# Optimization experiments

Hardware: AMD Instinct MI355X
Metric: run time of the kernel (lower is better)

## Reference

```python
import jax, jax.numpy as jnp
import numpy as np

B, T = 64, 512
E, F, NUM = 8, 64, 16          # num embedding features, per-feature emb dim, numeric feats
D = E * F + NUM                 # 528, input_dim
HE = 512                        # encoder_hidden
HD = 512                        # decoder_gru_hidden
V = 500                         # vocab per categorical feature


def setup_inputs() -> dict:
    key = jax.random.key(0)
    ks = jax.random.split(key, 32)
    se = 1.0 / np.sqrt(HE)
    sd = 1.0 / np.sqrt(HD)
    u = lambda k, shape, s: jax.random.uniform(k, shape, jnp.float32, -s, s)
    return dict(
        x=jax.random.normal(ks[0], (B, T, D), jnp.float32),
        # encoder nn.GRU params (gate order r,z,n)
        Wih=u(ks[1], (3 * HE, D), se), Whh=u(ks[2], (3 * HE, HE), se),
        bih=u(ks[3], (3 * HE,), se), bhh=u(ks[4], (3 * HE,), se),
        # decoder layer 0 (input_size=D)
        W0x=u(ks[5], (3 * HD, D), sd), b0x=u(ks[6], (3 * HD,), sd),
        W0h=u(ks[7], (3 * HD, HD), sd), b0h=u(ks[8], (3 * HD,), sd),
        W0m=u(ks[9], (HD, HE + HD), sd), b0m=u(ks[10], (HD,), sd),
        # decoder layer 1 (input_size=HD)
        W1x=u(ks[11], (3 * HD, HD), sd), b1x=u(ks[12], (3 * HD,), sd),
        W1h=u(ks[13], (3 * HD, HD), sd), b1h=u(ks[14], (3 * HD,), sd),
        W1m=u(ks[15], (HD, HE + HD), sd), b1m=u(ks[16], (HD,), sd),
        # output heads
        Wout=u(ks[17], (D, HD), sd), bout=u(ks[18], (D,), sd),
        Wdel=u(ks[19], (1, HD), sd), bdel=u(ks[20], (1,), sd),
        # stacked per-feature vocab heads: Linear(F, V) for each of E features
        Wemb=u(ks[21], (E, V, F), 1.0 / np.sqrt(F)), bemb=u(ks[22], (E, V), 1.0 / np.sqrt(F)),
        seq_lens=jax.random.randint(ks[23], (B,), 1, T + 1),
    )


def _gru_cell(xg, hg, hx):
    # xg, hg: [B, 3H] precomputed input/hidden projections; hx: mixed hidden
    xr, xz, xn = jnp.split(xg, 3, axis=-1)
    hr, hz, hn = jnp.split(hg, 3, axis=-1)
    r = jax.nn.sigmoid(xr + hr)
    z = jax.nn.sigmoid(xz + hz)
    n = jnp.tanh(xn + r * hn)
    return z * hx + (1.0 - z) * n  # custom GRUCell convention: hy = z*hx + (1-z)*n


def reference(x, Wih, Whh, bih, bhh, W0x, b0x, W0h, b0h, W0m, b0m,
              W1x, b1x, W1h, b1h, W1m, b1m, Wout, bout, Wdel, bdel,
              Wemb, bemb, seq_lens):
    Bc, Tc, Dc = x.shape
    # ---------------- encoder: standard nn.GRU ----------------
    xg_enc = jnp.einsum('btd,gd->tbg', x, Wih) + bih  # [T,B,3HE]

    def enc_step(h, xt):
        hg = h @ Whh.T + bhh
        xr, xz, xn = jnp.split(xt, 3, axis=-1)
        hr, hz, hn = jnp.split(hg, 3, axis=-1)
        r = jax.nn.sigmoid(xr + hr)
        z = jax.nn.sigmoid(xz + hz)
        n = jnp.tanh(xn + r * hn)
        h = (1.0 - z) * n + z * h  # torch nn.GRU convention
        return h, h

    _, hs = jax.lax.scan(enc_step, jnp.zeros((Bc, HE), x.dtype), xg_enc)  # hs: [T,B,HE]
    lens = jnp.clip(seq_lens - 1, 0, Tc - 1)
    last_hidden = hs[lens, jnp.arange(Bc)]  # == all_hid[:, lens].diagonal().T -> [B,HE]

    # ---------------- DecoderGRU with per-step global mixing ----------------
    x2h0 = jnp.einsum('btd,gd->tbg', x, W0x) + b0x  # [T,B,3HD]
    # mix_global(cat([global_hidden, hx])) : global part is constant over time
    ghm0 = last_hidden @ W0m[:, :HE].T + b0m  # [B,HD]
    ghm1 = last_hidden @ W1m[:, :HE].T + b1m
    W0mh = W0m[:, HE:]
    W1mh = W1m[:, HE:]

    def dec_step(carry, xg_t):
        h0, h1 = carry
        hx0 = ghm0 + h0 @ W0mh.T
        h0 = _gru_cell(xg_t, hx0 @ W0h.T + b0h, hx0)
        xg1 = h0 @ W1x.T + b1x
        hx1 = ghm1 + h1 @ W1mh.T
        h1 = _gru_cell(xg1, hx1 @ W1h.T + b1h, hx1)
        return (h0, h1), h1

    z0 = jnp.zeros((Bc, HD), x.dtype)
    _, dec = jax.lax.scan(dec_step, (z0, z0), x2h0)  # [T,B,HD]
    dec = dec.transpose(1, 0, 2)  # [B,T,HD]

    out = (dec @ Wout.T + bout)[:, :-1, :]              # [B,T-1,D]
    pred_delta = (dec @ Wdel.T + bdel)[:, :-1, 0]       # [B,T-1]
    resized = out[:, :, :E * F].reshape(Bc, Tc - 1, E, F)
    emb_logits = jnp.einsum('btef,evf->ebtv', resized, Wemb) + bemb[:, None, None, :]
    return out, pred_delta, emb_logits, last_hidden
```

## Files before the change

kernel.cpp:

```cpp
#include <hip/hip_runtime.h>
#include <stdint.h>

typedef unsigned short u16;
typedef __attribute__((ext_vector_type(8))) short short8;
typedef __attribute__((ext_vector_type(4))) float f32x4;

#define MFMA16(a,b,c) __builtin_amdgcn_mfma_f32_16x16x32_bf16((a),(b),(c),0,0,0)
#define AT_LD(p)    __hip_atomic_load((p), __ATOMIC_RELAXED, __HIP_MEMORY_SCOPE_AGENT)
#define AT_LD64(p)  __hip_atomic_load((p), __ATOMIC_RELAXED, __HIP_MEMORY_SCOPE_AGENT)
#define AT_ST(p,v)  __hip_atomic_store((p), (v), __ATOMIC_RELAXED, __HIP_MEMORY_SCOPE_AGENT)

__device__ __forceinline__ float b2f(u16 u){
  union { uint32_t i; float f; } v; v.i = ((uint32_t)u) << 16; return v.f;
}
__device__ __forceinline__ u16 f2bf(float f){
  union { float f; uint32_t i; } v; v.f = f;
  uint32_t x = v.i;
  return (u16)((x + 0x7fffu + ((x >> 16) & 1u)) >> 16);
}
__device__ __forceinline__ float sigm(float x){ return 1.f/(1.f + __expf(-x)); }
__device__ __forceinline__ float tanh_f(float x){ float e = __expf(-2.f*x); return 2.f/(1.f+e) - 1.f; }

__device__ __forceinline__ void gbar_arrive(unsigned* flags, int my, unsigned target){
  __syncthreads();
  if (threadIdx.x == 0) AT_ST(&flags[my*32], target);
}
__device__ __forceinline__ void gbar_wait16(unsigned* flags, unsigned target){
  if (threadIdx.x < 16){
    while (AT_LD(&flags[threadIdx.x*32]) < target) {}
  }
  __syncthreads();
}

__device__ __forceinline__ f32x4 xpose4(f32x4 a, int m){
  int b0 = m & 1, b1 = (m >> 1) & 1;
  float s01 = b0 ? a[0] : a[1];
  float s23 = b0 ? a[2] : a[3];
  float r01 = __shfl_xor(s01, 1);
  float r23 = __shfl_xor(s23, 1);
  float w0 = b0 ? r01 : a[0];
  float w1 = b0 ? a[1] : r01;
  float w2 = b0 ? r23 : a[2];
  float w3 = b0 ? a[3] : r23;
  float u02 = b1 ? w0 : w2;
  float u13 = b1 ? w1 : w3;
  float p02 = __shfl_xor(u02, 2);
  float p13 = __shfl_xor(u13, 2);
  f32x4 x;
  x[0] = b1 ? p02 : w0;
  x[1] = b1 ? p13 : w1;
  x[2] = b1 ? w2 : p02;
  x[3] = b1 ? w3 : p13;
  return x;
}

__device__ __forceinline__ void stage_h512(const u16* hrd, u16* hs, int tid){
  const unsigned long long* h64 = (const unsigned long long*)hrd;
  #pragma unroll
  for (int cc=0; cc<8; ++cc){
    int S = cc*512 + tid;
    int row = S >> 6, s = S & 63;
    union { unsigned long long q[2]; short8 v; } pk;
    pk.q[0] = AT_LD64(h64 + (size_t)S*2);
    pk.q[1] = AT_LD64(h64 + (size_t)S*2 + 1);
    *(short8*)&hs[row*512 + ((s ^ (row&7))<<3)] = pk.v;
  }
}
__device__ __forceinline__ void stage_h256(const u16* hrd, u16* hs, int tid){
  const unsigned long long* h64 = (const unsigned long long*)hrd;
  #pragma unroll
  for (int cc=0; cc<16; ++cc){
    int S = cc*256 + tid;
    int row = S >> 6, s = S & 63;
    union { unsigned long long q[2]; short8 v; } pk;
    pk.q[0] = AT_LD64(h64 + (size_t)S*2);
    pk.q[1] = AT_LD64(h64 + (size_t)S*2 + 1);
    *(short8*)&hs[row*512 + ((s ^ (row&7))<<3)] = pk.v;
  }
}

__global__ void cvt_pad(const float* __restrict__ src, u16* __restrict__ dst,
                        int R, int sStride, int sOff, int Cd, int Ccopy){
  int i = blockIdx.x*256 + threadIdx.x;
  if (i >= R*Cd) return;
  int r = i / Cd, c = i % Cd;
  dst[i] = (c < Ccopy) ? f2bf(src[(size_t)r*sStride + sOff + c]) : (u16)0;
}

__global__ void padf(const float* __restrict__ src, float* __restrict__ dst, int R, int Cs, int Cd){
  int i = blockIdx.x*256 + threadIdx.x;
  if (i >= R*Cd) return;
  int r = i/Cd, c = i%Cd;
  dst[i] = (c < Cs) ? src[r*Cs + c] : 0.f;
}

__global__ void wmT_kernel(const float* __restrict__ Wm, u16* __restrict__ dst){
  int idx = blockIdx.x*256 + threadIdx.x;
  if (idx >= 512*512) return;
  int j = idx >> 9, k = idx & 511;
  dst[idx] = f2bf(Wm[(size_t)k*1024 + 512 + j]);
}

__global__ __launch_bounds__(256) void gemm_bt(
    const u16* __restrict__ A, int lda,
    const u16* __restrict__ Bw, int ldb,
    const float* __restrict__ bias,
    int M, int N, int K, int mode,
    void* __restrict__ o0, void* __restrict__ o1, void* __restrict__ o2, int ldo)
{
  if (mode == 3){
    int e = blockIdx.z;
    A    += (size_t)e * 64;
    Bw   += (size_t)e * 512 * 64;
    bias += (size_t)e * 512;
  }
  __shared__ u16 As[128*64];
  __shared__ u16 Bs[128*64];
  const int row0 = blockIdx.x * 128, col0 = blockIdx.y * 128;
  const int tid = threadIdx.x;
  const int l = tid & 63, w = tid >> 6;
  const int lr = l & 15, lk = l >> 4;
  const int wr = w >> 1, wc = w & 1;
  f32x4 acc[4][4];
  #pragma unroll
  for (int a=0;a<4;++a)
    #pragma unroll
    for (int b=0;b<4;++b) acc[a][b] = (f32x4){0.f,0.f,0.f,0.f};

  for (int k0 = 0; k0 < K; k0 += 64){
    #pragma unroll
    for (int s = 0; s < 4; ++s){
      int cid = s*256 + tid;
      int r = cid >> 3, ck = cid & 7;
      *(short8*)&As[r*64 + ck*8] = *(const short8*)&A[(size_t)(row0 + r)*lda + k0 + ck*8];
      *(short8*)&Bs[r*64 + ck*8] = *(const short8*)&Bw[(size_t)(col0 + r)*ldb + k0 + ck*8];
    }
    __syncthreads();
    #pragma unroll
    for (int kt = 0; kt < 2; ++kt){
      short8 af[4], bf[4];
      #pragma unroll
      for (int mt=0;mt<4;++mt) af[mt] = *(const short8*)&As[(wr*64 + mt*16 + lr)*64 + kt*32 + lk*8];
      #pragma unroll
      for (int nt=0;nt<4;++nt) bf[nt] = *(const short8*)&Bs[(wc*64 + nt*16 + lr)*64 + kt*32 + lk*8];
      #pragma unroll
      for (int mt=0;mt<4;++mt)
        #pragma unroll
        for (int nt=0;nt<4;++nt) acc[mt][nt] = MFMA16(af[mt], bf[nt], acc[mt][nt]);
    }
    __syncthreads();
  }

  #pragma unroll
  for (int mt=0;mt<4;++mt){
    #pragma unroll
    for (int nt=0;nt<4;++nt){
      int col = col0 + wc*64 + nt*16 + lr;
      float bv = bias[col];
      #pragma unroll
      for (int i=0;i<4;++i){
        int r = row0 + wr*64 + mt*16 + lk*4 + i;
        float v = acc[mt][nt][i] + bv;
        if (mode == 0){
          int bb = r >> 9, t = r & 511;
          size_t ro = ((size_t)t*64 + bb)*1536;
          if (col < 1536) ((u16*)o0)[ro + col] = f2bf(v);
          else            ((u16*)o1)[ro + col - 1536] = f2bf(v);
        } else if (mode == 1){
          ((u16*)o0)[(size_t)r*ldo + col] = f2bf(v);
        } else if (mode == 2){
          int t = r >> 6, bb = r & 63;
          if (t < 511){
            size_t orow = (size_t)bb*511 + t;
            if (col < 512){
              ((float*)o0)[orow*528 + col] = v;
              ((u16*)o2)[orow*512 + col] = f2bf(v);
            } else if (col < 528){
              ((float*)o0)[orow*528 + col] = v;
            } else if (col == 528){
              ((float*)o1)[orow] = v;
            }
          }
        } else if (mode == 3){
          if (r < M && col < 500) ((float*)o0)[(size_t)(blockIdx.z)*16352000ull + (size_t)r*500 + col] = v;
        } else {
          if (r < M) ((float*)o0)[(size_t)r*ldo + col] = v;
        }
      }
    }
  }
}

__global__ __launch_bounds__(512,2) void enc_kernel(
    const u16* __restrict__ Whh, const float* __restrict__ bhh,
    const u16* __restrict__ XGE, const int* __restrict__ seqs,
    u16* __restrict__ hd, float* __restrict__ lasth,
    unsigned* __restrict__ flags)
{
  __shared__ u16 hs[64*512];
  const int tid = threadIdx.x;
  const int l = tid & 63, w = tid >> 6;
  const int lr = l & 15, lk = l >> 4;
  const int m = l & 3;
  const int gw = blockIdx.x*8 + w;
  const int hcol = gw*4 + (lr >> 2);

  const int msel = (m == 3) ? 0 : m;
  const u16* wbase = Whh + ((size_t)(msel*512) + hcol)*512;
  short8 bw[16];
  #pragma unroll
  for (int kt=0;kt<16;++kt) bw[kt] = *(const short8*)&wbase[kt*32 + lk*8];

  const float bhr = bhh[hcol], bhz = bhh[512+hcol], bhn = bhh[1024+hcol];
  int rowc[4]; int len[4]; float hreg[4];
  float xr[4], xz[4], xn[4];
  #pragma unroll
  for (int c=0;c<4;++c){
    rowc[c] = c*16 + lk*4 + m;
    len[c] = seqs[rowc[c]];
    hreg[c] = 0.f;
    const u16* p = XGE + (size_t)rowc[c]*1536;
    xr[c]=b2f(p[hcol]); xz[c]=b2f(p[512+hcol]); xn[c]=b2f(p[1024+hcol]);
  }

  for (int t=0; t<512; ++t){
    const u16* hrd = hd + (t & 1)*32768;
    u16*       hwr = hd + ((t & 1)^1)*32768;
    stage_h512(hrd, hs, tid);
    __syncthreads();
    #pragma unroll
    for (int c=0;c<4;++c){
      short8 af[16];
      #pragma unroll
      for (int kt=0;kt<16;++kt)
        af[kt] = *(const short8*)&hs[(c*16+lr)*512 + (((kt*4+lk) ^ (lr&7))<<3)];
      f32x4 acc = (f32x4){0.f,0.f,0.f,0.f};
      #pragma unroll
      for (int kt=0;kt<16;++kt) acc = MFMA16(af[kt], bw[kt], acc);
      f32x4 x = xpose4(acc, m);
      float rg = sigm(xr[c] + x[0] + bhr);
      float zg = sigm(xz[c] + x[1] + bhz);
      float ng = tanh_f(xn[c] + rg*(x[2] + bhn));
      float hv = (1.f - zg)*ng + zg*hreg[c];
      hreg[c] = hv;
      AT_ST(&hwr[rowc[c]*512 + hcol], f2bf(hv));
      if (t == len[c]-1) lasth[rowc[c]*512 + hcol] = hv;
    }
    if (t < 511){
      gbar_arrive(flags, blockIdx.x, (unsigned)(t+1));
      const u16* xgn = XGE + (size_t)(t+1)*98304;
      #pragma unroll
      for (int c=0;c<4;++c){
        const u16* p = xgn + (size_t)rowc[c]*1536;
        xr[c]=b2f(p[hcol]); xz[c]=b2f(p[512+hcol]); xn[c]=b2f(p[1024+hcol]);
      }
      gbar_wait16(flags, (unsigned)(t+1));
    }
  }
}

__global__ __launch_bounds__(256,1) void decf_kernel(
    const u16* __restrict__ Wm0, const u16* __restrict__ Wcp0,
    const float* __restrict__ ghm0v, const float* __restrict__ ghW0v,
    const u16* __restrict__ W1xc, const float* __restrict__ b1xv,
    const u16* __restrict__ Wm1, const u16* __restrict__ Wcp1,
    const float* __restrict__ ghm1v, const float* __restrict__ ghW1v,
    const u16* __restrict__ XG0,
    u16* __restrict__ h0d, u16* __restrict__ h1d,
    u16* __restrict__ xgb,
    u16* __restrict__ Hall,
    unsigned* __restrict__ flags)
{
  __shared__ u16 hs[64*512];
  const int tid = threadIdx.x;
  const int l = tid & 63, w = tid >> 6;
  const int lr = l & 15, lk = l >> 4;
  const int m = l & 3;
  const int role1 = (blockIdx.x >= 32) ? 1 : 0;
  const int b = blockIdx.x & 31;
  const int gw = b*4 + w;
  const int hcol = gw*4 + (lr >> 2);

  const u16* Wm  = role1 ? Wm1  : Wm0;
  const u16* Wcp = role1 ? Wcp1 : Wcp0;
  const float* ghm = role1 ? ghm1v : ghm0v;
  const float* ghW = role1 ? ghW1v : ghW0v;

  const u16* wb = (m == 0) ? (Wm + (size_t)hcol*512)
                           : (Wcp + ((size_t)((m-1)*512) + hcol)*512);
  short8 bw[16];
  #pragma unroll
  for (int kt=0;kt<16;++kt) bw[kt] = *(const short8*)&wb[kt*32 + lk*8];

  const bool xact = (!role1) && (gw < 96);
  const int xcol0 = gw*16;
  const int cbase = xcol0 + (lr & ~3);
  short8 bwx[16];
  float bx0=0.f, bx1=0.f, bx2=0.f, bx3=0.f;
  if (xact){
    #pragma unroll
    for (int kt=0;kt<16;++kt) bwx[kt] = *(const short8*)&W1xc[(size_t)(xcol0+lr)*512 + kt*32 + lk*8];
    bx0 = b1xv[cbase]; bx1 = b1xv[cbase+1]; bx2 = b1xv[cbase+2]; bx3 = b1xv[cbase+3];
  }

  int rowc[4]; float ghmr[4], g0[4], g1[4], g2[4];
  #pragma unroll
  for (int c=0;c<4;++c){
    int row = c*16 + lk*4 + m; rowc[c] = row;
    ghmr[c] = ghm[row*512 + hcol];
    g0[c] = ghW[row*1536 + hcol];
    g1[c] = ghW[row*1536 + 512 + hcol];
    g2[c] = ghW[row*1536 + 1024 + hcol];
  }
  float xr[4], xz[4], xn[4];
  if (!role1){
    #pragma unroll
    for (int c=0;c<4;++c){
      const u16* p = XG0 + (size_t)rowc[c]*1536;
      xr[c]=b2f(p[hcol]); xz[c]=b2f(p[512+hcol]); xn[c]=b2f(p[1024+hcol]);
    }
  } else {
    #pragma unroll
    for (int c=0;c<4;++c){ xr[c]=0.f; xz[c]=0.f; xn[c]=0.f; }
  }

  for (int p=0; p<=513; ++p){
    if (!role1){
      if (p <= 512){
        const int sp = p & 1;
        const u16* hrd = h0d + sp*32768;
        u16*       hwr = h0d + (sp^1)*32768;
        stage_h256(hrd, hs, tid);
        __syncthreads();
        #pragma unroll
        for (int c=0;c<4;++c){
          short8 af[16];
          #pragma unroll
          for (int kt=0;kt<16;++kt)
            af[kt] = *(const short8*)&hs[(c*16+lr)*512 + (((kt*4+lk) ^ (lr&7))<<3)];
          if (p <= 511){
            f32x4 ga = (f32x4){0.f,0.f,0.f,0.f};
            #pragma unroll
            for (int kt=0;kt<16;++kt) ga = MFMA16(af[kt], bw[kt], ga);
            f32x4 x = xpose4(ga, m);
            float hx = x[0] + ghmr[c];
            float rv = sigm(xr[c] + x[1] + g0[c]);
            float zv = sigm(xz[c] + x[2] + g1[c]);
            float nv = tanh_f(xn[c] + rv*(x[3] + g2[c]));
            float hv = zv*hx + (1.f - zv)*nv;
            AT_ST(&hwr[rowc[c]*512 + hcol], f2bf(hv));
          }
          if (p >= 1 && xact){
            u16* xw = xgb + (size_t)((p-1)%3)*98304;
            f32x4 xa = (f32x4){0.f,0.f,0.f,0.f};
            #pragma unroll
            for (int kt=0;kt<16;++kt) xa = MFMA16(af[kt], bwx[kt], xa);
            f32x4 xv = xpose4(xa, m);
            unsigned lo = (unsigned)f2bf(xv[0]+bx0) | ((unsigned)f2bf(xv[1]+bx1) << 16);
            unsigned hi = (unsigned)f2bf(xv[2]+bx2) | ((unsigned)f2bf(xv[3]+bx3) << 16);
            unsigned long long v64 = (unsigned long long)lo | ((unsigned long long)hi << 32);
            __hip_atomic_store((unsigned long long*)&xw[(size_t)rowc[c]*1536 + cbase], v64,
                               __ATOMIC_RELAXED, __HIP_MEMORY_SCOPE_AGENT);
          }
        }
      }
    } else {
      if (p >= 2){
        const int t = p - 2;
        const u16* xb = xgb + (size_t)(t%3)*98304;
        #pragma unroll
        for (int c=0;c<4;++c){
          xr[c] = b2f(AT_LD(&xb[(size_t)rowc[c]*1536 + hcol]));
          xz[c] = b2f(AT_LD(&xb[(size_t)rowc[c]*1536 + 512 + hcol]));
          xn[c] = b2f(AT_LD(&xb[(size_t)rowc[c]*1536 + 1024 + hcol]));
        }
        const u16* hrd = h1d + (t&1)*32768;
        u16*       hwr = h1d + ((t&1)^1)*32768;
        stage_h256(hrd, hs, tid);
        __syncthreads();
        #pragma unroll
        for (int c=0;c<4;++c){
          short8 af[16];
          #pragma unroll
          for (int kt=0;kt<16;++kt)
            af[kt] = *(const short8*)&hs[(c*16+lr)*512 + (((kt*4+lk) ^ (lr&7))<<3)];
          f32x4 ga = (f32x4){0.f,0.f,0.f,0.f};
          #pragma unroll
          for (int kt=0;kt<16;++kt) ga = MFMA16(af[kt], bw[kt], ga);
          f32x4 x = xpose4(ga, m);
          float hx = x[0] + ghmr[c];
          float rv = sigm(xr[c] + x[1] + g0[c]);
          float zv = sigm(xz[c] + x[2] + g1[c]);
          float nv = tanh_f(xn[c] + rv*(x[3] + g2[c]));
          float hv = zv*hx + (1.f - zv)*nv;
          u16 hb = f2bf(hv);
          AT_ST(&hwr[rowc[c]*512 + hcol], hb);
          Hall[(size_t)t*32768 + rowc[c]*512 + hcol] = hb;
        }
      }
    }
    if (p < 513){
      __syncthreads();
      if (tid == 0) AT_ST(&flags[blockIdx.x*32], (unsigned)(p+1));
      if (!role1 && p <= 510){
        const u16* xgn = XG0 + (size_t)(p+1)*98304;
        #pragma unroll
        for (int c=0;c<4;++c){
          const u16* q = xgn + (size_t)rowc[c]*1536;
          xr[c]=b2f(q[hcol]); xz[c]=b2f(q[512+hcol]); xn[c]=b2f(q[1024+hcol]);
        }
      }
      if (!role1){
        if (tid < 32){
          while (AT_LD(&flags[tid*32]) < (unsigned)(p+1)) {}
        } else if (tid < 64){
          if (p >= 1){ while (AT_LD(&flags[tid*32]) < (unsigned)p) {} }
        }
      } else {
        if (tid < 64){
          while (AT_LD(&flags[tid*32]) < (unsigned)(p+1)) {}
        }
      }
      __syncthreads();
    }
  }
}

__global__ void ghm_kernel(const float* __restrict__ lasth,
                           const float* __restrict__ W0m, const float* __restrict__ b0m,
                           const float* __restrict__ W1m, const float* __restrict__ b1m,
                           float* __restrict__ ghm0, float* __restrict__ ghm1,
                           u16* __restrict__ ghmP)
{
  int idx = blockIdx.x*256 + threadIdx.x;
  int chain = idx >> 15;
  int j = (idx >> 6) & 511;
  int b = idx & 63;
  const float* Wm = chain ? W1m : W0m;
  const float* bm = chain ? b1m : b0m;
  float s = 0.f;
  for (int k=0;k<512;++k) s += lasth[b*512 + k] * Wm[(size_t)j*1024 + k];
  float v = s + bm[j];
  (chain ? ghm1 : ghm0)[b*512 + j] = v;
  ghmP[(size_t)chain*65536 + b*512 + j] = f2bf(v);
}

extern "C" void kernel_launch(void* const* d_in, const int* in_sizes, int n_in,
                              void* d_out, int out_size, void* d_ws, size_t ws_size,
                              hipStream_t stream)
{
  const float* x    = (const float*)d_in[0];
  const float* Wih  = (const float*)d_in[1];
  const float* Whh  = (const float*)d_in[2];
  const float* bih  = (const float*)d_in[3];
  const float* bhh  = (const float*)d_in[4];
  const float* W0x  = (const float*)d_in[5];
  const float* b0x  = (const float*)d_in[6];
  const float* W0h  = (const float*)d_in[7];
  const float* b0h  = (const float*)d_in[8];
  const float* W0m  = (const float*)d_in[9];
  const float* b0m  = (const float*)d_in[10];
  const float* W1x  = (const float*)d_in[11];
  const float* b1x  = (const float*)d_in[12];
  const float* W1h  = (const float*)d_in[13];
  const float* b1h  = (const float*)d_in[14];
  const float* W1m  = (const float*)d_in[15];
  const float* b1m  = (const float*)d_in[16];
  const float* Wout = (const float*)d_in[17];
  const float* bout = (const float*)d_in[18];
  const float* Wdel = (const float*)d_in[19];
  const float* bdel = (const float*)d_in[20];
  const float* Wemb = (const float*)d_in[21];
  const float* bemb = (const float*)d_in[22];
  const int*   seqs = (const int*)d_in[23];
  float* out = (float*)d_out;

  const size_t OFF_DELTA = 17267712ull;
  const size_t OFF_EMB   = 17300416ull;
  const size_t OFF_LASTH = 148116416ull;

  uint8_t* ws = (uint8_t*)d_ws;
  size_t off = 0;
  auto alloc = [&](size_t bytes)->size_t{ size_t p = off; off += (bytes + 511) & ~(size_t)511; return p; };
  u16*   XGE  = (u16*)(ws + alloc(32768ull*1536*2));
  u16*   WmT0 = XGE;
  u16*   WmT1 = XGE + 262144;
  u16*   XG0  = (u16*)(ws + alloc(32768ull*1536*2));
  u16*   Ob   = XG0;
  uint8_t* reg3 = ws + alloc(2ull*33554432);
  u16*   Xp   = (u16*)reg3;
  u16*   H1   = (u16*)reg3;
  u16*   Wc   = (u16*)(ws + alloc(3072ull*576*2));
  u16*   Whc  = (u16*)(ws + alloc(1536ull*512*2));
  u16*   W0hc = (u16*)(ws + alloc(1536ull*512*2));
  u16*   W1hc = (u16*)(ws + alloc(1536ull*512*2));
  u16*   W1xc = (u16*)(ws + alloc(1536ull*512*2));
  u16*   Wm0c = (u16*)(ws + alloc(512ull*512*2));
  u16*   Wm1c = (u16*)(ws + alloc(512ull*512*2));
  u16*   Wcp0 = (u16*)(ws + alloc(1536ull*512*2));
  u16*   Wcp1 = (u16*)(ws + alloc(1536ull*512*2));
  u16*   Woc  = (u16*)(ws + alloc(640ull*512*2));
  u16*   Wep  = (u16*)(ws + alloc(8ull*512*64*2));
  u16*   ghmP = (u16*)(ws + alloc(2ull*128*512*2));
  u16*   xgb  = (u16*)(ws + alloc(3ull*64*1536*2));
  float* bc1  = (float*)(ws + alloc(3072*4));
  float* bc3  = (float*)(ws + alloc(640*4));
  float* bep  = (float*)(ws + alloc(8*512*4));
  float* bzero= (float*)(ws + alloc(512*4));
  float* ghm0 = (float*)(ws + alloc(64*512*4));
  float* ghm1 = (float*)(ws + alloc(64*512*4));
  float* ghW0 = (float*)(ws + alloc(64*1536*4));
  float* ghW1 = (float*)(ws + alloc(64*1536*4));
  size_t state_off = off;
  u16*   henc = (u16*)(ws + alloc(2*64*512*2));
  u16*   h0d  = (u16*)(ws + alloc(2*64*512*2));
  u16*   h1d  = (u16*)(ws + alloc(2*64*512*2));
  unsigned* bars = (unsigned*)(ws + alloc(16384));
  size_t state_bytes = off - state_off;
  if (ws_size < off) return;

  hipMemsetAsync(ws + state_off, 0, state_bytes, stream);
  hipMemsetAsync(Woc, 0, 640ull*512*2, stream);
  hipMemsetAsync(Wep, 0, 8ull*512*64*2, stream);
  hipMemsetAsync(ghmP, 0, 2ull*128*512*2, stream);
  hipMemsetAsync(bc3, 0, 640*4, stream);
  hipMemsetAsync(bzero, 0, 512*4, stream);

  hipMemcpyAsync(bc1,        bih,  1536*4, hipMemcpyDeviceToDevice, stream);
  hipMemcpyAsync(bc1 + 1536, b0x,  1536*4, hipMemcpyDeviceToDevice, stream);
  hipMemcpyAsync(bc3,        bout, 528*4,  hipMemcpyDeviceToDevice, stream);
  hipMemcpyAsync(bc3 + 528,  bdel, 4,      hipMemcpyDeviceToDevice, stream);

  auto CV = [&](const float* s, u16* d, int R, int sStride, int sOff, int Cd, int Ccopy){
    int total = R*Cd; int gb = (total + 255)/256;
    cvt_pad<<<dim3(gb), dim3(256), 0, stream>>>(s, d, R, sStride, sOff, Cd, Ccopy);
  };
  CV(x,    Xp, 32768, 528, 0, 576, 528);
  CV(Wih,  Wc,              1536, 528, 0, 576, 528);
  CV(W0x,  Wc + 1536ull*576,1536, 528, 0, 576, 528);
  CV(Whh,  Whc,  1536, 512, 0, 512, 512);
  CV(W0h,  W0hc, 1536, 512, 0, 512, 512);
  CV(W1h,  W1hc, 1536, 512, 0, 512, 512);
  CV(W1x,  W1xc, 1536, 512, 0, 512, 512);
  CV(W0m,  Wm0c, 512, 1024, 512, 512, 512);
  CV(W1m,  Wm1c, 512, 1024, 512, 512, 512);
  CV(Wout, Woc,              528, 512, 0, 512, 512);
  CV(Wdel, Woc + 528ull*512, 1,   512, 0, 512, 512);
  for (int e=0;e<8;++e) CV(Wemb + (size_t)e*32000, Wep + (size_t)e*32768, 500, 64, 0, 64, 64);
  {
    int gb = (8*512 + 255)/256;
    padf<<<dim3(gb), dim3(256), 0, stream>>>(bemb, bep, 8, 500, 512);
  }
  wmT_kernel<<<dim3(1024), dim3(256), 0, stream>>>(W0m, WmT0);
  wmT_kernel<<<dim3(1024), dim3(256), 0, stream>>>(W1m, WmT1);

  gemm_bt<<<dim3(12,4), dim3(256), 0, stream>>>(W0hc, 512, WmT0, 512, bzero,
      1536, 512, 512, 1, Wcp0, nullptr, nullptr, 512);
  gemm_bt<<<dim3(12,4), dim3(256), 0, stream>>>(W1hc, 512, WmT1, 512, bzero,
      1536, 512, 512, 1, Wcp1, nullptr, nullptr, 512);

  gemm_bt<<<dim3(256,24), dim3(256), 0, stream>>>(Xp, 576, Wc, 576, bc1,
      32768, 3072, 576, 0, XGE, XG0, nullptr, 0);
  enc_kernel<<<dim3(16), dim3(512), 0, stream>>>(Whc, bhh, XGE, seqs,
      henc, out + OFF_LASTH, bars + 0);
  ghm_kernel<<<dim3(256), dim3(256), 0, stream>>>(out + OFF_LASTH, W0m, b0m, W1m, b1m,
      ghm0, ghm1, ghmP);
  gemm_bt<<<dim3(1,12), dim3(256), 0, stream>>>(ghmP, 512, W0hc, 512, b0h,
      64, 1536, 512, 5, ghW0, nullptr, nullptr, 1536);
  gemm_bt<<<dim3(1,12), dim3(256), 0, stream>>>(ghmP + 65536, 512, W1hc, 512, b1h,
      64, 1536, 512, 5, ghW1, nullptr, nullptr, 1536);
  decf_kernel<<<dim3(64), dim3(256), 0, stream>>>(
      Wm0c, Wcp0, ghm0, ghW0, W1xc, b1x,
      Wm1c, Wcp1, ghm1, ghW1,
      XG0, h0d, h1d, xgb, H1, bars + 1024);
  gemm_bt<<<dim3(256,5), dim3(256), 0, stream>>>(H1, 512, Woc, 512, bc3,
      32768, 640, 512, 2, out, out + OFF_DELTA, Ob, 0);
  gemm_bt<<<dim3(256,4,8), dim3(256), 0, stream>>>(Ob, 512, Wep, 64, bep,
      32704, 512, 64, 3, out + OFF_EMB, nullptr, nullptr, 0);
}
```

Before: 8.276 ms.

## Overlap decoder input projection GEMM with encoder recurrence; shrink layer-1 decoder blocks

The decoder layer-0 input projection (XG0) is split out of the big input GEMM and computed by extra blocks launched alongside the 16 persistent encoder recurrence blocks in one kernel. This lets that GEMM run on otherwise idle CUs while the latency-bound encoder loop runs. Separately, the decoder layer-1 role now uses 16 blocks that each handle two hidden-column groups instead of 32 blocks handling one, so the barrier covers 48 blocks instead of 64. The xgb ring-buffer index is also re-expressed. The risk is that the GEMM blocks may be scheduled ahead of the encoder blocks or compete with them for resources, and that layer-1 blocks now do twice the work per step.

```diff
diff --git a/kernel.cpp b/kernel.cpp
--- a/kernel.cpp
+++ b/kernel.cpp
@@ -191,70 +191,133 @@
   }
 }
 
-__global__ __launch_bounds__(512,2) void enc_kernel(
+__global__ __launch_bounds__(512,2) void encg_kernel(
     const u16* __restrict__ Whh, const float* __restrict__ bhh,
     const u16* __restrict__ XGE, const int* __restrict__ seqs,
     u16* __restrict__ hd, float* __restrict__ lasth,
-    unsigned* __restrict__ flags)
+    unsigned* __restrict__ flags,
+    const u16* __restrict__ Xp, const u16* __restrict__ Wcx,
+    const float* __restrict__ biasx, u16* __restrict__ XG0)
 {
-  __shared__ u16 hs[64*512];
+  __shared__ u16 shbuf[64*512];
   const int tid = threadIdx.x;
-  const int l = tid & 63, w = tid >> 6;
-  const int lr = l & 15, lk = l >> 4;
-  const int m = l & 3;
-  const int gw = blockIdx.x*8 + w;
-  const int hcol = gw*4 + (lr >> 2);
-
-  const int msel = (m == 3) ? 0 : m;
-  const u16* wbase = Whh + ((size_t)(msel*512) + hcol)*512;
-  short8 bw[16];
-  #pragma unroll
-  for (int kt=0;kt<16;++kt) bw[kt] = *(const short8*)&wbase[kt*32 + lk*8];
-
-  const float bhr = bhh[hcol], bhz = bhh[512+hcol], bhn = bhh[1024+hcol];
-  int rowc[4]; int len[4]; float hreg[4];
-  float xr[4], xz[4], xn[4];
-  #pragma unroll
-  for (int c=0;c<4;++c){
-    rowc[c] = c*16 + lk*4 + m;
-    len[c] = seqs[rowc[c]];
-    hreg[c] = 0.f;
-    const u16* p = XGE + (size_t)rowc[c]*1536;
-    xr[c]=b2f(p[hcol]); xz[c]=b2f(p[512+hcol]); xn[c]=b2f(p[1024+hcol]);
-  }
-
-  for (int t=0; t<512; ++t){
-    const u16* hrd = hd + (t & 1)*32768;
-    u16*       hwr = hd + ((t & 1)^1)*32768;
-    stage_h512(hrd, hs, tid);
-    __syncthreads();
+  if (blockIdx.x < 16){
+    u16* hs = shbuf;
+    const int l = tid & 63, w = tid >> 6;
+    const int lr = l & 15, lk = l >> 4;
+    const int m = l & 3;
+    const int gw = blockIdx.x*8 + w;
+    const int hcol = gw*4 + (lr >> 2);
+
+    const int msel = (m == 3) ? 0 : m;
+    const u16* wbase = Whh + ((size_t)(msel*512) + hcol)*512;
+    short8 bw[16];
+    #pragma unroll
+    for (int kt=0;kt<16;++kt) bw[kt] = *(const short8*)&wbase[kt*32 + lk*8];
+
+    const float bhr = bhh[hcol], bhz = bhh[512+hcol], bhn = bhh[1024+hcol];
+    int rowc[4]; int len[4]; float hreg[4];
+    float xr[4], xz[4], xn[4];
     #pragma unroll
     for (int c=0;c<4;++c){
-      short8 af[16];
-      #pragma unroll
-      for (int kt=0;kt<16;++kt)
-        af[kt] = *(const short8*)&hs[(c*16+lr)*512 + (((kt*4+lk) ^ (lr&7))<<3)];
-      f32x4 acc = (f32x4){0.f,0.f,0.f,0.f};
-      #pragma unroll
-      for (int kt=0;kt<16;++kt) acc = MFMA16(af[kt], bw[kt], acc);
-      f32x4 x = xpose4(acc, m);
-      float rg = sigm(xr[c] + x[0] + bhr);
-      float zg = sigm(xz[c] + x[1] + bhz);
-      float ng = tanh_f(xn[c] + rg*(x[2] + bhn));
-      float hv = (1.f - zg)*ng + zg*hreg[c];
-      hreg[c] = hv;
-      AT_ST(&hwr[rowc[c]*512 + hcol], f2bf(hv));
-      if (t == len[c]-1) lasth[rowc[c]*512 + hcol] = hv;
-    }
-    if (t < 511){
-      gbar_arrive(flags, blockIdx.x, (unsigned)(t+1));
-      const u16* xgn = XGE + (size_t)(t+1)*98304;
+      rowc[c] = c*16 + lk*4 + m;
+      len[c] = seqs[rowc[c]];
+      hreg[c] = 0.f;
+      const u16* p = XGE + (size_t)rowc[c]*1536;
+      xr[c]=b2f(p[hcol]); xz[c]=b2f(p[512+hcol]); xn[c]=b2f(p[1024+hcol]);
+    }
+
+    for (int t=0; t<512; ++t){
+      const u16* hrd = hd + (t & 1)*32768;
+      u16*       hwr = hd + ((t & 1)^1)*32768;
+      stage_h512(hrd, hs, tid);
+      __syncthreads();
       #pragma unroll
       for (int c=0;c<4;++c){
-        const u16* p = xgn + (size_t)rowc[c]*1536;
-        xr[c]=b2f(p[hcol]); xz[c]=b2f(p[512+hcol]); xn[c]=b2f(p[1024+hcol]);
-      }
-      gbar_wait16(flags, (unsigned)(t+1));
+        short8 af[16];
+        #pragma unroll
+        for (int kt=0;kt<16;++kt)
+          af[kt] = *(const short8*)&hs[(c*16+lr)*512 + (((kt*4+lk) ^ (lr&7))<<3)];
+        f32x4 acc = (f32x4){0.f,0.f,0.f,0.f};
+        #pragma unroll
+        for (int kt=0;kt<16;++kt) acc = MFMA16(af[kt], bw[kt], acc);
+        f32x4 x = xpose4(acc, m);
+        float rg = sigm(xr[c] + x[0] + bhr);
+        float zg = sigm(xz[c] + x[1] + bhz);
+        float ng = tanh_f(xn[c] + rg*(x[2] + bhn));
+        float hv = (1.f - zg)*ng + zg*hreg[c];
+        hreg[c] = hv;
+        AT_ST(&hwr[rowc[c]*512 + hcol], f2bf(hv));
+        if (t == len[c]-1) lasth[rowc[c]*512 + hcol] = hv;
+      }
+      if (t < 511){
+        gbar_arrive(flags, blockIdx.x, (unsigned)(t+1));
+        const u16* p0 = XGE + (size_t)(t+1)*98304;
+        #pragma unroll
+        for (int c=0;c<4;++c){
+          const u16* p = p0 + (size_t)rowc[c]*1536;
+          xr[c]=b2f(p[hcol]); xz[c]=b2f(p[512+hcol]); xn[c]=b2f(p[1024+hcol]);
+        }
+        gbar_wait16(flags, (unsigned)(t+1));
+      }
+    }
+  } else {
+    const int g = blockIdx.x - 16;
+    const int row0 = (g & 255)*128, col0 = (g >> 8)*128;
+    const bool act = tid < 256;
+    u16* As = shbuf;
+    u16* Bs = shbuf + 8192;
+    const int l = tid & 63, w = tid >> 6;
+    const int lr = l & 15, lk = l >> 4;
+    const int wr = (w & 3) >> 1, wc = w & 1;
+    f32x4 acc[4][4];
+    #pragma unroll
+    for (int a=0;a<4;++a)
+      #pragma unroll
+      for (int b=0;b<4;++b) acc[a][b] = (f32x4){0.f,0.f,0.f,0.f};
+
+    for (int k0 = 0; k0 < 576; k0 += 64){
+      if (act){
+        #pragma unroll
+        for (int s = 0; s < 4; ++s){
+          int cid = s*256 + tid;
+          int r = cid >> 3, ck = cid & 7;
+          *(short8*)&As[r*64 + ck*8] = *(const short8*)&Xp[(size_t)(row0 + r)*576 + k0 + ck*8];
+          *(short8*)&Bs[r*64 + ck*8] = *(const short8*)&Wcx[(size_t)(col0 + r)*576 + k0 + ck*8];
+        }
+      }
+      __syncthreads();
+      if (act){
+        #pragma unroll
+        for (int kt = 0; kt < 2; ++kt){
+          short8 af[4], bf[4];
+          #pragma unroll
+          for (int mt=0;mt<4;++mt) af[mt] = *(const short8*)&As[(wr*64 + mt*16 + lr)*64 + kt*32 + lk*8];
+          #pragma unroll
+          for (int nt=0;nt<4;++nt) bf[nt] = *(const short8*)&Bs[(wc*64 + nt*16 + lr)*64 + kt*32 + lk*8];
+          #pragma unroll
+          for (int mt=0;mt<4;++mt)
+            #pragma unroll
+            for (int nt=0;nt<4;++nt) acc[mt][nt] = MFMA16(af[mt], bf[nt], acc[mt][nt]);
+        }
+      }
+      __syncthreads();
+    }
+    if (act){
+      #pragma unroll
+      for (int mt=0;mt<4;++mt){
+        #pragma unroll
+        for (int nt=0;nt<4;++nt){
+          int col = col0 + wc*64 + nt*16 + lr;
+          float bv = biasx[col];
+          #pragma unroll
+          for (int i=0;i<4;++i){
+            int r = row0 + wr*64 + mt*16 + lk*4 + i;
+            int bb = r >> 9, t = r & 511;
+            XG0[((size_t)t*64 + bb)*1536 + col] = f2bf(acc[mt][nt][i] + bv);
+          }
+        }
+      }
     }
   }
 }
@@ -276,62 +339,49 @@
   const int l = tid & 63, w = tid >> 6;
   const int lr = l & 15, lk = l >> 4;
   const int m = l & 3;
-  const int role1 = (blockIdx.x >= 32) ? 1 : 0;
-  const int b = blockIdx.x & 31;
-  const int gw = b*4 + w;
-  const int hcol = gw*4 + (lr >> 2);
-
-  const u16* Wm  = role1 ? Wm1  : Wm0;
-  const u16* Wcp = role1 ? Wcp1 : Wcp0;
-  const float* ghm = role1 ? ghm1v : ghm0v;
-  const float* ghW = role1 ? ghW1v : ghW0v;
-
-  const u16* wb = (m == 0) ? (Wm + (size_t)hcol*512)
-                           : (Wcp + ((size_t)((m-1)*512) + hcol)*512);
-  short8 bw[16];
+
+  int rowc[4];
   #pragma unroll
-  for (int kt=0;kt<16;++kt) bw[kt] = *(const short8*)&wb[kt*32 + lk*8];
-
-  const bool xact = (!role1) && (gw < 96);
-  const int xcol0 = gw*16;
-  const int cbase = xcol0 + (lr & ~3);
-  short8 bwx[16];
-  float bx0=0.f, bx1=0.f, bx2=0.f, bx3=0.f;
-  if (xact){
-    #pragma unroll
-    for (int kt=0;kt<16;++kt) bwx[kt] = *(const short8*)&W1xc[(size_t)(xcol0+lr)*512 + kt*32 + lk*8];
-    bx0 = b1xv[cbase]; bx1 = b1xv[cbase+1]; bx2 = b1xv[cbase+2]; bx3 = b1xv[cbase+3];
-  }
-
-  int rowc[4]; float ghmr[4], g0[4], g1[4], g2[4];
-  #pragma unroll
-  for (int c=0;c<4;++c){
-    int row = c*16 + lk*4 + m; rowc[c] = row;
-    ghmr[c] = ghm[row*512 + hcol];
-    g0[c] = ghW[row*1536 + hcol];
-    g1[c] = ghW[row*1536 + 512 + hcol];
-    g2[c] = ghW[row*1536 + 1024 + hcol];
-  }
-  float xr[4], xz[4], xn[4];
-  if (!role1){
+  for (int c=0;c<4;++c) rowc[c] = c*16 + lk*4 + m;
+
+  if (blockIdx.x < 32){
+    const int gw = blockIdx.x*4 + w;
+    const int hcol = gw*4 + (lr >> 2);
+    const u16* wb = (m == 0) ? (Wm0 + (size_t)hcol*512)
+                             : (Wcp0 + ((size_t)((m-1)*512) + hcol)*512);
+    short8 bw[16];
+    #pragma unroll
+    for (int kt=0;kt<16;++kt) bw[kt] = *(const short8*)&wb[kt*32 + lk*8];
+
+    const bool xact = (gw < 96);
+    const int xcol0 = gw*16;
+    const int cbase = xcol0 + (lr & ~3);
+    short8 bwx[16];
+    float bx0=0.f, bx1=0.f, bx2=0.f, bx3=0.f;
+    if (xact){
+      #pragma unroll
+      for (int kt=0;kt<16;++kt) bwx[kt] = *(const short8*)&W1xc[(size_t)(xcol0+lr)*512 + kt*32 + lk*8];
+      bx0 = b1xv[cbase]; bx1 = b1xv[cbase+1]; bx2 = b1xv[cbase+2]; bx3 = b1xv[cbase+3];
+    }
+    float ghmr[4], g0[4], g1[4], g2[4];
+    float xr[4], xz[4], xn[4];
     #pragma unroll
     for (int c=0;c<4;++c){
-      const u16* p = XG0 + (size_t)rowc[c]*1536;
+      int row = rowc[c];
+      ghmr[c] = ghm0v[row*512 + hcol];
+      g0[c] = ghW0v[row*1536 + hcol];
+      g1[c] = ghW0v[row*1536 + 512 + hcol];
+      g2[c] = ghW0v[row*1536 + 1024 + hcol];
+      const u16* p = XG0 + (size_t)row*1536;
       xr[c]=b2f(p[hcol]); xz[c]=b2f(p[512+hcol]); xn[c]=b2f(p[1024+hcol]);
     }
-  } else {
-    #pragma unroll
-    for (int c=0;c<4;++c){ xr[c]=0.f; xz[c]=0.f; xn[c]=0.f; }
-  }
-
-  for (int p=0; p<=513; ++p){
-    if (!role1){
+
+    for (int p=0; p<=513; ++p){
       if (p <= 512){
-        const int sp = p & 1;
-        const u16* hrd = h0d + sp*32768;
-        u16*       hwr = h0d + (sp^1)*32768;
-        stage_h256(hrd, hs, tid);
+        stage_h256(h0d + (p&1)*32768, hs, tid);
         __syncthreads();
+        u16* hwr = h0d + ((p&1)^1)*32768;
+        u16* xw  = xgb + (size_t)((p+2)%3)*98304;
         #pragma unroll
         for (int c=0;c<4;++c){
           short8 af[16];
@@ -351,7 +401,6 @@
             AT_ST(&hwr[rowc[c]*512 + hcol], f2bf(hv));
           }
           if (p >= 1 && xact){
-            u16* xw = xgb + (size_t)((p-1)%3)*98304;
             f32x4 xa = (f32x4){0.f,0.f,0.f,0.f};
             #pragma unroll
             for (int kt=0;kt<16;++kt) xa = MFMA16(af[kt], bwx[kt], xa);
@@ -364,64 +413,98 @@
           }
         }
       }
-    } else {
+      if (p < 513){
+        __syncthreads();
+        if (tid == 0) AT_ST(&flags[blockIdx.x*32], (unsigned)(p+1));
+        if (p <= 510){
+          const u16* xgn = XG0 + (size_t)(p+1)*98304;
+          #pragma unroll
+          for (int c=0;c<4;++c){
+            const u16* q = xgn + (size_t)rowc[c]*1536;
+            xr[c]=b2f(q[hcol]); xz[c]=b2f(q[512+hcol]); xn[c]=b2f(q[1024+hcol]);
+          }
+        }
+        if (tid < 32){
+          while (AT_LD(&flags[tid*32]) < (unsigned)(p+1)) {}
+        } else if (tid < 48){
+          while (AT_LD(&flags[tid*32]) < (unsigned)p) {}
+        }
+        __syncthreads();
+      }
+    }
+  } else {
+    const int gw = (blockIdx.x - 32)*4 + w;
+    int hc2[2];
+    hc2[0] = gw*8 + (lr >> 2);
+    hc2[1] = gw*8 + 4 + (lr >> 2);
+    short8 bw1[2][16];
+    #pragma unroll
+    for (int h=0;h<2;++h){
+      const u16* wb = (m == 0) ? (Wm1 + (size_t)hc2[h]*512)
+                               : (Wcp1 + ((size_t)((m-1)*512) + hc2[h])*512);
+      #pragma unroll
+      for (int kt=0;kt<16;++kt) bw1[h][kt] = *(const short8*)&wb[kt*32 + lk*8];
+    }
+    float ghmr[2][4], g0[2][4], g1[2][4], g2[2][4];
+    #pragma unroll
+    for (int h=0;h<2;++h)
+      #pragma unroll
+      for (int c=0;c<4;++c){
+        int row = rowc[c];
+        ghmr[h][c] = ghm1v[row*512 + hc2[h]];
+        g0[h][c] = ghW1v[row*1536 + hc2[h]];
+        g1[h][c] = ghW1v[row*1536 + 512 + hc2[h]];
+        g2[h][c] = ghW1v[row*1536 + 1024 + hc2[h]];
+      }
+
+    for (int p=0; p<=513; ++p){
       if (p >= 2){
         const int t = p - 2;
         const u16* xb = xgb + (size_t)(t%3)*98304;
-        #pragma unroll
-        for (int c=0;c<4;++c){
-          xr[c] = b2f(AT_LD(&xb[(size_t)rowc[c]*1536 + hcol]));
-          xz[c] = b2f(AT_LD(&xb[(size_t)rowc[c]*1536 + 512 + hcol]));
-          xn[c] = b2f(AT_LD(&xb[(size_t)rowc[c]*1536 + 1024 + hcol]));
-        }
-        const u16* hrd = h1d + (t&1)*32768;
-        u16*       hwr = h1d + ((t&1)^1)*32768;
-        stage_h256(hrd, hs, tid);
+        float xr[2][4], xz[2][4], xn[2][4];
+        #pragma unroll
+        for (int h=0;h<2;++h)
+          #pragma unroll
+          for (int c=0;c<4;++c){
+            xr[h][c] = b2f(AT_LD(&xb[(size_t)rowc[c]*1536 + hc2[h]]));
+            xz[h][c] = b2f(AT_LD(&xb[(size_t)rowc[c]*1536 + 512 + hc2[h]]));
+            xn[h][c] = b2f(AT_LD(&xb[(size_t)rowc[c]*1536 + 1024 + hc2[h]]));
+          }
+        stage_h256(h1d + (t&1)*32768, hs, tid);
         __syncthreads();
+        u16* hwr = h1d + ((t&1)^1)*32768;
+        u16* Ht  = Hall + (size_t)t*32768;
         #pragma unroll
         for (int c=0;c<4;++c){
           short8 af[16];
           #pragma unroll
           for (int kt=0;kt<16;++kt)
             af[kt] = *(const short8*)&hs[(c*16+lr)*512 + (((kt*4+lk) ^ (lr&7))<<3)];
-          f32x4 ga = (f32x4){0.f,0.f,0.f,0.f};
-          #pragma unroll
-          for (int kt=0;kt<16;++kt) ga = MFMA16(af[kt], bw[kt], ga);
-          f32x4 x = xpose4(ga, m);
-          float hx = x[0] + ghmr[c];
-          float rv = sigm(xr[c] + x[1] + g0[c]);
-          float zv = sigm(xz[c] + x[2] + g1[c]);
-          float nv = tanh_f(xn[c] + rv*(x[3] + g2[c]));
-          float hv = zv*hx + (1.f - zv)*nv;
-          u16 hb = f2bf(hv);
-          AT_ST(&hwr[rowc[c]*512 + hcol], hb);
-          Hall[(size_t)t*32768 + rowc[c]*512 + hcol] = hb;
-        }
-      }
-    }
-    if (p < 513){
-      __syncthreads();
-      if (tid == 0) AT_ST(&flags[blockIdx.x*32], (unsigned)(p+1));
-      if (!role1 && p <= 510){
-        const u16* xgn = XG0 + (size_t)(p+1)*98304;
-        #pragma unroll
-        for (int c=0;c<4;++c){
-          const u16* q = xgn + (size_t)rowc[c]*1536;
-          xr[c]=b2f(q[hcol]); xz[c]=b2f(q[512+hcol]); xn[c]=b2f(q[1024+hcol]);
-        }
-      }
-      if (!role1){
-        if (tid < 32){
+          #pragma unroll
+          for (int h=0;h<2;++h){
+            f32x4 ga = (f32x4){0.f,0.f,0.f,0.f};
+            #pragma unroll
+            for (int kt=0;kt<16;++kt) ga = MFMA16(af[kt], bw1[h][kt], ga);
+            f32x4 x = xpose4(ga, m);
+            float hx = x[0] + ghmr[h][c];
+            float rv = sigm(xr[h][c] + x[1] + g0[h][c]);
+            float zv = sigm(xz[h][c] + x[2] + g1[h][c]);
+            float nv = tanh_f(xn[h][c] + rv*(x[3] + g2[h][c]));
+            float hv = zv*hx + (1.f - zv)*nv;
+            u16 hb = f2bf(hv);
+            AT_ST(&hwr[rowc[c]*512 + hc2[h]], hb);
+            Ht[rowc[c]*512 + hc2[h]] = hb;
+          }
+        }
+      }
+      if (p < 513){
+        __syncthreads();
+        if (tid == 0) AT_ST(&flags[blockIdx.x*32], (unsigned)(p+1));
+        if (tid < 48){
           while (AT_LD(&flags[tid*32]) < (unsigned)(p+1)) {}
-        } else if (tid < 64){
-          if (p >= 1){ while (AT_LD(&flags[tid*32]) < (unsigned)p) {} }
-        }
-      } else {
-        if (tid < 64){
-          while (AT_LD(&flags[tid*32]) < (unsigned)(p+1)) {}
-        }
-      }
-      __syncthreads();
+        }
+        __syncthreads();
+      }
     }
   }
 }
@@ -559,17 +642,18 @@
   gemm_bt<<<dim3(12,4), dim3(256), 0, stream>>>(W1hc, 512, WmT1, 512, bzero,
       1536, 512, 512, 1, Wcp1, nullptr, nullptr, 512);
 
-  gemm_bt<<<dim3(256,24), dim3(256), 0, stream>>>(Xp, 576, Wc, 576, bc1,
-      32768, 3072, 576, 0, XGE, XG0, nullptr, 0);
-  enc_kernel<<<dim3(16), dim3(512), 0, stream>>>(Whc, bhh, XGE, seqs,
-      henc, out + OFF_LASTH, bars + 0);
+  gemm_bt<<<dim3(256,12), dim3(256), 0, stream>>>(Xp, 576, Wc, 576, bc1,
+      32768, 1536, 576, 0, XGE, nullptr, nullptr, 0);
+  encg_kernel<<<dim3(16 + 3072), dim3(512), 0, stream>>>(Whc, bhh, XGE, seqs,
+      henc, out + OFF_LASTH, bars + 0,
+      Xp, Wc + 1536ull*576, bc1 + 1536, XG0);
   ghm_kernel<<<dim3(256), dim3(256), 0, stream>>>(out + OFF_LASTH, W0m, b0m, W1m, b1m,
       ghm0, ghm1, ghmP);
   gemm_bt<<<dim3(1,12), dim3(256), 0, stream>>>(ghmP, 512, W0hc, 512, b0h,
       64, 1536, 512, 5, ghW0, nullptr, nullptr, 1536);
   gemm_bt<<<dim3(1,12), dim3(256), 0, stream>>>(ghmP + 65536, 512, W1hc, 512, b1h,
       64, 1536, 512, 5, ghW1, nullptr, nullptr, 1536);
-  decf_kernel<<<dim3(64), dim3(256), 0, stream>>>(
+  decf_kernel<<<dim3(48), dim3(256), 0, stream>>>(
       Wm0c, Wcp0, ghm0, ghW0, W1xc, b1x,
       Wm1c, Wcp1, ghm1, ghW1,
       XG0, h0d, h1d, xgb, H1, bars + 1024);
```

Measured after the change: 9.295 ms. 1.12x slower.

## Overlap decoder input projection GEMM with encoder recurrence in one launch

Applied to the files above, without the earlier changes.

The input-projection GEMM previously produced both the encoder and decoder gate inputs before the serial encoder ran. Now only the encoder half is computed up front. The decoder half (XG0) is computed by 3072 extra blocks appended to the encoder kernel launch, so it can run on idle CUs while the 16 persistent encoder blocks step through time. The risk is that the extra blocks compete with the latency-bound recurrence for memory bandwidth and scheduling. The encoder's grid barrier also assumes its 16 blocks are co-resident, which depends on the hardware dispatching them first.

```diff
diff --git a/kernel.cpp b/kernel.cpp
--- a/kernel.cpp
+++ b/kernel.cpp
@@ -191,70 +191,133 @@
   }
 }
 
-__global__ __launch_bounds__(512,2) void enc_kernel(
+__global__ __launch_bounds__(512,2) void encg_kernel(
     const u16* __restrict__ Whh, const float* __restrict__ bhh,
     const u16* __restrict__ XGE, const int* __restrict__ seqs,
     u16* __restrict__ hd, float* __restrict__ lasth,
-    unsigned* __restrict__ flags)
+    unsigned* __restrict__ flags,
+    const u16* __restrict__ Xp, const u16* __restrict__ Wcx,
+    const float* __restrict__ biasx, u16* __restrict__ XG0)
 {
-  __shared__ u16 hs[64*512];
+  __shared__ u16 shbuf[64*512];
   const int tid = threadIdx.x;
-  const int l = tid & 63, w = tid >> 6;
-  const int lr = l & 15, lk = l >> 4;
-  const int m = l & 3;
-  const int gw = blockIdx.x*8 + w;
-  const int hcol = gw*4 + (lr >> 2);
-
-  const int msel = (m == 3) ? 0 : m;
-  const u16* wbase = Whh + ((size_t)(msel*512) + hcol)*512;
-  short8 bw[16];
-  #pragma unroll
-  for (int kt=0;kt<16;++kt) bw[kt] = *(const short8*)&wbase[kt*32 + lk*8];
-
-  const float bhr = bhh[hcol], bhz = bhh[512+hcol], bhn = bhh[1024+hcol];
-  int rowc[4]; int len[4]; float hreg[4];
-  float xr[4], xz[4], xn[4];
-  #pragma unroll
-  for (int c=0;c<4;++c){
-    rowc[c] = c*16 + lk*4 + m;
-    len[c] = seqs[rowc[c]];
-    hreg[c] = 0.f;
-    const u16* p = XGE + (size_t)rowc[c]*1536;
-    xr[c]=b2f(p[hcol]); xz[c]=b2f(p[512+hcol]); xn[c]=b2f(p[1024+hcol]);
-  }
-
-  for (int t=0; t<512; ++t){
-    const u16* hrd = hd + (t & 1)*32768;
-    u16*       hwr = hd + ((t & 1)^1)*32768;
-    stage_h512(hrd, hs, tid);
-    __syncthreads();
+  if (blockIdx.x < 16){
+    u16* hs = shbuf;
+    const int l = tid & 63, w = tid >> 6;
+    const int lr = l & 15, lk = l >> 4;
+    const int m = l & 3;
+    const int gw = blockIdx.x*8 + w;
+    const int hcol = gw*4 + (lr >> 2);
+
+    const int msel = (m == 3) ? 0 : m;
+    const u16* wbase = Whh + ((size_t)(msel*512) + hcol)*512;
+    short8 bw[16];
+    #pragma unroll
+    for (int kt=0;kt<16;++kt) bw[kt] = *(const short8*)&wbase[kt*32 + lk*8];
+
+    const float bhr = bhh[hcol], bhz = bhh[512+hcol], bhn = bhh[1024+hcol];
+    int rowc[4]; int len[4]; float hreg[4];
+    float xr[4], xz[4], xn[4];
     #pragma unroll
     for (int c=0;c<4;++c){
-      short8 af[16];
-      #pragma unroll
-      for (int kt=0;kt<16;++kt)
-        af[kt] = *(const short8*)&hs[(c*16+lr)*512 + (((kt*4+lk) ^ (lr&7))<<3)];
-      f32x4 acc = (f32x4){0.f,0.f,0.f,0.f};
-      #pragma unroll
-      for (int kt=0;kt<16;++kt) acc = MFMA16(af[kt], bw[kt], acc);
-      f32x4 x = xpose4(acc, m);
-      float rg = sigm(xr[c] + x[0] + bhr);
-      float zg = sigm(xz[c] + x[1] + bhz);
-      float ng = tanh_f(xn[c] + rg*(x[2] + bhn));
-      float hv = (1.f - zg)*ng + zg*hreg[c];
-      hreg[c] = hv;
-      AT_ST(&hwr[rowc[c]*512 + hcol], f2bf(hv));
-      if (t == len[c]-1) lasth[rowc[c]*512 + hcol] = hv;
-    }
-    if (t < 511){
-      gbar_arrive(flags, blockIdx.x, (unsigned)(t+1));
-      const u16* xgn = XGE + (size_t)(t+1)*98304;
+      rowc[c] = c*16 + lk*4 + m;
+      len[c] = seqs[rowc[c]];
+      hreg[c] = 0.f;
+      const u16* p = XGE + (size_t)rowc[c]*1536;
+      xr[c]=b2f(p[hcol]); xz[c]=b2f(p[512+hcol]); xn[c]=b2f(p[1024+hcol]);
+    }
+
+    for (int t=0; t<512; ++t){
+      const u16* hrd = hd + (t & 1)*32768;
+      u16*       hwr = hd + ((t & 1)^1)*32768;
+      stage_h512(hrd, hs, tid);
+      __syncthreads();
       #pragma unroll
       for (int c=0;c<4;++c){
-        const u16* p = xgn + (size_t)rowc[c]*1536;
-        xr[c]=b2f(p[hcol]); xz[c]=b2f(p[512+hcol]); xn[c]=b2f(p[1024+hcol]);
-      }
-      gbar_wait16(flags, (unsigned)(t+1));
+        short8 af[16];
+        #pragma unroll
+        for (int kt=0;kt<16;++kt)
+          af[kt] = *(const short8*)&hs[(c*16+lr)*512 + (((kt*4+lk) ^ (lr&7))<<3)];
+        f32x4 acc = (f32x4){0.f,0.f,0.f,0.f};
+        #pragma unroll
+        for (int kt=0;kt<16;++kt) acc = MFMA16(af[kt], bw[kt], acc);
+        f32x4 x = xpose4(acc, m);
+        float rg = sigm(xr[c] + x[0] + bhr);
+        float zg = sigm(xz[c] + x[1] + bhz);
+        float ng = tanh_f(xn[c] + rg*(x[2] + bhn));
+        float hv = (1.f - zg)*ng + zg*hreg[c];
+        hreg[c] = hv;
+        AT_ST(&hwr[rowc[c]*512 + hcol], f2bf(hv));
+        if (t == len[c]-1) lasth[rowc[c]*512 + hcol] = hv;
+      }
+      if (t < 511){
+        gbar_arrive(flags, blockIdx.x, (unsigned)(t+1));
+        const u16* p0 = XGE + (size_t)(t+1)*98304;
+        #pragma unroll
+        for (int c=0;c<4;++c){
+          const u16* p = p0 + (size_t)rowc[c]*1536;
+          xr[c]=b2f(p[hcol]); xz[c]=b2f(p[512+hcol]); xn[c]=b2f(p[1024+hcol]);
+        }
+        gbar_wait16(flags, (unsigned)(t+1));
+      }
+    }
+  } else {
+    const int g = blockIdx.x - 16;
+    const int row0 = (g & 255)*128, col0 = (g >> 8)*128;
+    const bool act = tid < 256;
+    u16* As = shbuf;
+    u16* Bs = shbuf + 8192;
+    const int l = tid & 63, w = tid >> 6;
+    const int lr = l & 15, lk = l >> 4;
+    const int wr = (w & 3) >> 1, wc = w & 1;
+    f32x4 acc[4][4];
+    #pragma unroll
+    for (int a=0;a<4;++a)
+      #pragma unroll
+      for (int b=0;b<4;++b) acc[a][b] = (f32x4){0.f,0.f,0.f,0.f};
+
+    for (int k0 = 0; k0 < 576; k0 += 64){
+      if (act){
+        #pragma unroll
+        for (int s = 0; s < 4; ++s){
+          int cid = s*256 + tid;
+          int r = cid >> 3, ck = cid & 7;
+          *(short8*)&As[r*64 + ck*8] = *(const short8*)&Xp[(size_t)(row0 + r)*576 + k0 + ck*8];
+          *(short8*)&Bs[r*64 + ck*8] = *(const short8*)&Wcx[(size_t)(col0 + r)*576 + k0 + ck*8];
+        }
+      }
+      __syncthreads();
+      if (act){
+        #pragma unroll
+        for (int kt = 0; kt < 2; ++kt){
+          short8 af[4], bf[4];
+          #pragma unroll
+          for (int mt=0;mt<4;++mt) af[mt] = *(const short8*)&As[(wr*64 + mt*16 + lr)*64 + kt*32 + lk*8];
+          #pragma unroll
+          for (int nt=0;nt<4;++nt) bf[nt] = *(const short8*)&Bs[(wc*64 + nt*16 + lr)*64 + kt*32 + lk*8];
+          #pragma unroll
+          for (int mt=0;mt<4;++mt)
+            #pragma unroll
+            for (int nt=0;nt<4;++nt) acc[mt][nt] = MFMA16(af[mt], bf[nt], acc[mt][nt]);
+        }
+      }
+      __syncthreads();
+    }
+    if (act){
+      #pragma unroll
+      for (int mt=0;mt<4;++mt){
+        #pragma unroll
+        for (int nt=0;nt<4;++nt){
+          int col = col0 + wc*64 + nt*16 + lr;
+          float bv = biasx[col];
+          #pragma unroll
+          for (int i=0;i<4;++i){
+            int r = row0 + wr*64 + mt*16 + lk*4 + i;
+            int bb = r >> 9, t = r & 511;
+            XG0[((size_t)t*64 + bb)*1536 + col] = f2bf(acc[mt][nt][i] + bv);
+          }
+        }
+      }
     }
   }
 }
@@ -328,10 +391,9 @@
     if (!role1){
       if (p <= 512){
         const int sp = p & 1;
-        const u16* hrd = h0d + sp*32768;
-        u16*       hwr = h0d + (sp^1)*32768;
-        stage_h256(hrd, hs, tid);
+        stage_h256(h0d + sp*32768, hs, tid);
         __syncthreads();
+        u16* hwr = h0d + (sp^1)*32768;
         #pragma unroll
         for (int c=0;c<4;++c){
           short8 af[16];
@@ -351,7 +413,7 @@
             AT_ST(&hwr[rowc[c]*512 + hcol], f2bf(hv));
           }
           if (p >= 1 && xact){
-            u16* xw = xgb + (size_t)((p-1)%3)*98304;
+            u16* xw = xgb + (size_t)((p+2)%3)*98304;
             f32x4 xa = (f32x4){0.f,0.f,0.f,0.f};
             #pragma unroll
             for (int kt=0;kt<16;++kt) xa = MFMA16(af[kt], bwx[kt], xa);
@@ -374,10 +436,9 @@
           xz[c] = b2f(AT_LD(&xb[(size_t)rowc[c]*1536 + 512 + hcol]));
           xn[c] = b2f(AT_LD(&xb[(size_t)rowc[c]*1536 + 1024 + hcol]));
         }
-        const u16* hrd = h1d + (t&1)*32768;
-        u16*       hwr = h1d + ((t&1)^1)*32768;
-        stage_h256(hrd, hs, tid);
+        stage_h256(h1d + (t&1)*32768, hs, tid);
         __syncthreads();
+        u16* hwr = h1d + ((t&1)^1)*32768;
         #pragma unroll
         for (int c=0;c<4;++c){
           short8 af[16];
@@ -559,10 +620,11 @@
   gemm_bt<<<dim3(12,4), dim3(256), 0, stream>>>(W1hc, 512, WmT1, 512, bzero,
       1536, 512, 512, 1, Wcp1, nullptr, nullptr, 512);
 
-  gemm_bt<<<dim3(256,24), dim3(256), 0, stream>>>(Xp, 576, Wc, 576, bc1,
-      32768, 3072, 576, 0, XGE, XG0, nullptr, 0);
-  enc_kernel<<<dim3(16), dim3(512), 0, stream>>>(Whc, bhh, XGE, seqs,
-      henc, out + OFF_LASTH, bars + 0);
+  gemm_bt<<<dim3(256,12), dim3(256), 0, stream>>>(Xp, 576, Wc, 576, bc1,
+      32768, 1536, 576, 0, XGE, nullptr, nullptr, 0);
+  encg_kernel<<<dim3(16 + 3072), dim3(512), 0, stream>>>(Whc, bhh, XGE, seqs,
+      henc, out + OFF_LASTH, bars + 0,
+      Xp, Wc + 1536ull*576, bc1 + 1536, XG0);
   ghm_kernel<<<dim3(256), dim3(256), 0, stream>>>(out + OFF_LASTH, W0m, b0m, W1m, b1m,
       ghm0, ghm1, ghmP);
   gemm_bt<<<dim3(1,12), dim3(256), 0, stream>>>(ghmP, 512, W0hc, 512, b0h,
```

Measured after the change: 8.187 ms, median of 2. Within noise of the previous version (-1.1%).
